# Performance work log

Measured on AMD Instinct MI355X. Metric: run time of the kernel, lower is better.

The kernel has to match this reference:

```python
import jax, jax.numpy as jnp
import numpy as np

B, T, I, H, O = 256, 100, 1024, 2048, 10

def setup_inputs() -> dict:
    key = jax.random.key(0)
    k = jax.random.split(key, 6)
    return {
        "x": jax.random.normal(k[0], (B, T, I), dtype=jnp.float32),
        "h0": jax.random.normal(k[1], (B, H), dtype=jnp.float32),
        "Win": jax.random.uniform(k[2], (I, H), dtype=jnp.float32, minval=-0.1, maxval=0.1),
        "W": jax.random.normal(k[3], (H, H), dtype=jnp.float32) * 0.01,
        "lin_w": jax.random.normal(k[4], (O, H), dtype=jnp.float32) * 0.02,
        "lin_b": jax.random.normal(k[5], (O,), dtype=jnp.float32) * 0.02,
    }

def reference(x, h0, Win, W, lin_w, lin_b):
    xin = jnp.einsum('bti,ih->bth', x, Win)  # precompute input projection for all steps

    def step(h, xin_t):
        h = jnp.tanh(xin_t + h @ W)
        y = h @ lin_w.T + lin_b
        return h, y

    _, ys = jax.lax.scan(step, h0, jnp.swapaxes(xin, 0, 1))  # ys: [T, B, O]
    return jnp.swapaxes(ys, 0, 1)  # [B, T, O]
```

## Files before the change

### kernel.cpp

```cpp
#include <hip/hip_runtime.h>
#include <math.h>

#define Bn 256
#define Tn 100
#define In 1024
#define Hn 2048
#define On 10
#define Kc (In + Hn)

typedef short s8v  __attribute__((ext_vector_type(8)));
typedef unsigned short us4 __attribute__((ext_vector_type(4)));
typedef float f32x4 __attribute__((ext_vector_type(4)));

__device__ __forceinline__ unsigned short f2bf(float f) {
    unsigned int u = __float_as_uint(f);
    u += 0x7fffu + ((u >> 16) & 1u);
    return (unsigned short)(u >> 16);
}


__global__ void conv_x_kernel(const float4* __restrict__ src, ushort4* __restrict__ dst) {
    int i = blockIdx.x * 256 + threadIdx.x;
    float4 v = src[i];
    ushort4 o;
    o.x = f2bf(v.x); o.y = f2bf(v.y); o.z = f2bf(v.z); o.w = f2bf(v.w);
    dst[i] = o;
}

__global__ void transpose_bf16_kernel(const float* __restrict__ src, unsigned short* __restrict__ dst,
                                      int N, int ld, int colOff) {
    __shared__ float tile[32][33];
    int k0 = blockIdx.x * 32;
    int n0 = blockIdx.y * 32;
    int c = threadIdx.x & 31;
    int r = threadIdx.x >> 5;
    #pragma unroll
    for (int i = 0; i < 32; i += 8)
        tile[r + i][c] = src[(size_t)(k0 + r + i) * N + n0 + c];
    __syncthreads();
    #pragma unroll
    for (int i = 0; i < 32; i += 8)
        dst[(size_t)(n0 + r + i) * ld + colOff + k0 + c] = f2bf(tile[c][r + i]);
}

__global__ void small_conv_kernel(const float* __restrict__ h0, const float* __restrict__ lin_w,
                                  unsigned short* __restrict__ h_all0, unsigned short* __restrict__ lwb,
                                  unsigned int* __restrict__ bar) {
    int idx = blockIdx.x * 256 + threadIdx.x;
    if (idx < 512) bar[idx] = 0u;
    if (idx < Bn * Hn) {
        h_all0[idx] = f2bf(h0[idx]);
    } else {
        int j = idx - Bn * Hn;
        int o = j >> 11;
        int k = j & 2047;
        lwb[j] = (o < On) ? f2bf(lin_w[o * Hn + k]) : (unsigned short)0;
    }
}

__global__ __launch_bounds__(512, 2)
void scan_kernel(const unsigned short* __restrict__ xb,
                 const unsigned short* __restrict__ BTm,
                 unsigned short* __restrict__ h_all,
                 unsigned int* __restrict__ bar) {
    const int g = blockIdx.x;
    const int m0 = ((g >> 3) & 3) * 64;
    const int n0 = ((g & 7) * 8 + (g >> 5)) * 32;
    const int w = threadIdx.x >> 6;
    const int lane = threadIdx.x & 63;
    const int quad = lane >> 4;
    const int lr = lane & 15;

    __shared__ float red[4][64][36];

    const unsigned short* bp0 = BTm + (size_t)(n0 + lr) * Kc;
    const unsigned short* bp1 = BTm + (size_t)(n0 + 16 + lr) * Kc;

    const int kbase = w * 384;
    const size_t xrow = (size_t)Tn * In;

    unsigned int* grp_cnt = bar + (g & 7) * 32;
    unsigned int* mst_cnt = bar + 256;
    unsigned int* epoch   = bar + 288;

    for (int t = 0; t < Tn; ++t) {
        f32x4 acc[4][2];
        #pragma unroll
        for (int mi = 0; mi < 4; ++mi)
            #pragma unroll
            for (int ni = 0; ni < 2; ++ni)
                acc[mi][ni] = (f32x4){0.f, 0.f, 0.f, 0.f};

        const unsigned short* hprev = h_all + (size_t)t * (Bn * Hn);
        const unsigned short* xt = xb + (size_t)t * In;

        #pragma unroll
        for (int kk = 0; kk < 12; ++kk) {
            const int k0 = kbase + kk * 32;
            const int kq = k0 + quad * 8;
            const unsigned short* ab;
            size_t rstr;
            if (k0 < In) { ab = xt + kq; rstr = xrow; }
            else         { ab = hprev + (kq - In); rstr = Hn; }
            const unsigned short* arow = ab + (size_t)(m0 + lr) * rstr;
            s8v a0 = *(const s8v*)(arow);
            s8v a1 = *(const s8v*)(arow + 16 * rstr);
            s8v a2 = *(const s8v*)(arow + 32 * rstr);
            s8v a3 = *(const s8v*)(arow + 48 * rstr);
            s8v b0 = *(const s8v*)(bp0 + kq);
            s8v b1 = *(const s8v*)(bp1 + kq);
            acc[0][0] = __builtin_amdgcn_mfma_f32_16x16x32_bf16(a0, b0, acc[0][0], 0, 0, 0);
            acc[1][0] = __builtin_amdgcn_mfma_f32_16x16x32_bf16(a1, b0, acc[1][0], 0, 0, 0);
            acc[2][0] = __builtin_amdgcn_mfma_f32_16x16x32_bf16(a2, b0, acc[2][0], 0, 0, 0);
            acc[3][0] = __builtin_amdgcn_mfma_f32_16x16x32_bf16(a3, b0, acc[3][0], 0, 0, 0);
            acc[0][1] = __builtin_amdgcn_mfma_f32_16x16x32_bf16(a0, b1, acc[0][1], 0, 0, 0);
            acc[1][1] = __builtin_amdgcn_mfma_f32_16x16x32_bf16(a1, b1, acc[1][1], 0, 0, 0);
            acc[2][1] = __builtin_amdgcn_mfma_f32_16x16x32_bf16(a2, b1, acc[2][1], 0, 0, 0);
            acc[3][1] = __builtin_amdgcn_mfma_f32_16x16x32_bf16(a3, b1, acc[3][1], 0, 0, 0);
        }

        if (w < 4) {
            #pragma unroll
            for (int mi = 0; mi < 4; ++mi)
                #pragma unroll
                for (int ni = 0; ni < 2; ++ni)
                    #pragma unroll
                    for (int rr = 0; rr < 4; ++rr)
                        red[w][mi * 16 + quad * 4 + rr][ni * 16 + lr] = acc[mi][ni][rr];
        }
        __syncthreads();
        if (w >= 4) {
            #pragma unroll
            for (int mi = 0; mi < 4; ++mi)
                #pragma unroll
                for (int ni = 0; ni < 2; ++ni)
                    #pragma unroll
                    for (int rr = 0; rr < 4; ++rr)
                        red[w - 4][mi * 16 + quad * 4 + rr][ni * 16 + lr] += acc[mi][ni][rr];
        }
        __syncthreads();

        {
            int j = threadIdx.x << 2;
            int row = j >> 5;
            int c0 = j & 31;
            float4 s0 = *(const float4*)&red[0][row][c0];
            float4 s1 = *(const float4*)&red[1][row][c0];
            float4 s2 = *(const float4*)&red[2][row][c0];
            float4 s3 = *(const float4*)&red[3][row][c0];
            us4 o4;
            o4[0] = f2bf(tanhf(s0.x + s1.x + s2.x + s3.x));
            o4[1] = f2bf(tanhf(s0.y + s1.y + s2.y + s3.y));
            o4[2] = f2bf(tanhf(s0.z + s1.z + s2.z + s3.z));
            o4[3] = f2bf(tanhf(s0.w + s1.w + s2.w + s3.w));
            unsigned long long* dst = (unsigned long long*)
                (h_all + (size_t)(t + 1) * (Bn * Hn) + (size_t)(m0 + row) * Hn + n0 + c0);
            __hip_atomic_store(dst, __builtin_bit_cast(unsigned long long, o4),
                               __ATOMIC_RELAXED, __HIP_MEMORY_SCOPE_AGENT);
        }

        if (t < Tn - 1) {
            __syncthreads();
            if (threadIdx.x == 0) {
                const unsigned int tp1 = (unsigned int)(t + 1);
                unsigned int old = __hip_atomic_fetch_add(grp_cnt, 1u, __ATOMIC_RELAXED,
                                                          __HIP_MEMORY_SCOPE_AGENT);
                if (old == 32u * tp1 - 1u) {
                    unsigned int mo = __hip_atomic_fetch_add(mst_cnt, 1u, __ATOMIC_RELAXED,
                                                             __HIP_MEMORY_SCOPE_AGENT);
                    if (mo == 8u * tp1 - 1u)
                        __hip_atomic_store(epoch, tp1, __ATOMIC_RELAXED,
                                           __HIP_MEMORY_SCOPE_AGENT);
                }
                while (__hip_atomic_load(epoch, __ATOMIC_RELAXED,
                                         __HIP_MEMORY_SCOPE_AGENT) < tp1)
                    __builtin_amdgcn_s_sleep(4);
            }
            __syncthreads();
        }
    }
}

__global__ __launch_bounds__(256)
void gemm2_kernel(const unsigned short* __restrict__ h_all, const unsigned short* __restrict__ lwb,
                  const float* __restrict__ lb, float* __restrict__ y) {
    int gw = blockIdx.x * 4 + (threadIdx.x >> 6);
    int lane = threadIdx.x & 63, quad = lane >> 4, lr = lane & 15;
    int m0 = gw * 16;
    int t = m0 >> 8;
    int b0 = m0 & 255;
    const unsigned short* ah = h_all + ((size_t)(t + 1) * Bn + b0 + lr) * Hn + quad * 8;
    const unsigned short* bh = lwb + (size_t)lr * Hn + quad * 8;
    f32x4 acc0 = {0.f, 0.f, 0.f, 0.f}, acc1 = {0.f, 0.f, 0.f, 0.f};
    #pragma unroll
    for (int k0 = 0; k0 < Hn; k0 += 64) {
        s8v a0 = *(const s8v*)(ah + k0);
        s8v b0 = *(const s8v*)(bh + k0);
        acc0 = __builtin_amdgcn_mfma_f32_16x16x32_bf16(a0, b0, acc0, 0, 0, 0);
        s8v a1 = *(const s8v*)(ah + k0 + 32);
        s8v b1 = *(const s8v*)(bh + k0 + 32);
        acc1 = __builtin_amdgcn_mfma_f32_16x16x32_bf16(a1, b1, acc1, 0, 0, 0);
    }
    acc0 = acc0 + acc1;
    if (lr < On) {
        float bias = lb[lr];
        #pragma unroll
        for (int rr = 0; rr < 4; ++rr) {
            int b = b0 + quad * 4 + rr;
            y[(size_t)b * (Tn * On) + t * On + lr] = acc0[rr] + bias;
        }
    }
}


extern "C" void kernel_launch(void* const* d_in, const int* in_sizes, int n_in,
                              void* d_out, int out_size, void* d_ws, size_t ws_size,
                              hipStream_t stream) {
    const float* x   = (const float*)d_in[0];
    const float* h0  = (const float*)d_in[1];
    const float* Win = (const float*)d_in[2];
    const float* W   = (const float*)d_in[3];
    const float* lw  = (const float*)d_in[4];
    const float* lb  = (const float*)d_in[5];
    float* y = (float*)d_out;

    unsigned short* ws    = (unsigned short*)d_ws;
    unsigned short* xb    = ws;
    unsigned short* BTm   = xb + (size_t)Bn * Tn * In;
    unsigned short* h_all = BTm + (size_t)Hn * Kc;
    unsigned short* lwb   = h_all + (size_t)(Tn + 1) * Bn * Hn;
    unsigned int*   bar   = (unsigned int*)(lwb + 32768);

    conv_x_kernel<<<25600, 256, 0, stream>>>((const float4*)x, (ushort4*)xb);
    transpose_bf16_kernel<<<dim3(32, 64), 256, 0, stream>>>(Win, BTm, Hn, Kc, 0);
    transpose_bf16_kernel<<<dim3(64, 64), 256, 0, stream>>>(W, BTm, Hn, Kc, In);
    small_conv_kernel<<<2176, 256, 0, stream>>>(h0, lw, h_all, lwb, bar);

    scan_kernel<<<256, 512, 0, stream>>>(xb, BTm, h_all, bar);

    gemm2_kernel<<<400, 256, 0, stream>>>(h_all, lwb, lb, y);
}
```

Measured before the change: 1.564 ms.

## Keep weights in registers and overlap next-step input projection with barrier wait

Loads each warp's slice of the concatenated weight matrix into registers once, before the time loop, instead of reloading it every step. The K split is re-partitioned so each warp handles 128 x-columns and 256 h-columns. The x_t·Win contribution for the next step is computed before the grid barrier, so it is not on the serial critical path after the wait. The spin sleep is also shortened. The cost is a large increase in register use (96 extra VGPRs for weights), which may spill or limit occupancy under launch_bounds(512,2).

```diff
diff --git a/kernel.cpp b/kernel.cpp
--- a/kernel.cpp
+++ b/kernel.cpp
@@ -76,47 +76,73 @@
     const unsigned short* bp0 = BTm + (size_t)(n0 + lr) * Kc;
     const unsigned short* bp1 = BTm + (size_t)(n0 + 16 + lr) * Kc;
 
-    const int kbase = w * 384;
     const size_t xrow = (size_t)Tn * In;
 
     unsigned int* grp_cnt = bar + (g & 7) * 32;
     unsigned int* mst_cnt = bar + 256;
     unsigned int* epoch   = bar + 288;
 
+    s8v bx[4][2];
+    s8v bh[8][2];
+    #pragma unroll
+    for (int c = 0; c < 4; ++c) {
+        const int kq = w * 128 + c * 32 + quad * 8;
+        bx[c][0] = *(const s8v*)(bp0 + kq);
+        bx[c][1] = *(const s8v*)(bp1 + kq);
+    }
+    #pragma unroll
+    for (int c = 0; c < 8; ++c) {
+        const int kq = In + w * 256 + c * 32 + quad * 8;
+        bh[c][0] = *(const s8v*)(bp0 + kq);
+        bh[c][1] = *(const s8v*)(bp1 + kq);
+    }
+
+    f32x4 acc[4][2];
+    #pragma unroll
+    for (int mi = 0; mi < 4; ++mi)
+        #pragma unroll
+        for (int ni = 0; ni < 2; ++ni)
+            acc[mi][ni] = (f32x4){0.f, 0.f, 0.f, 0.f};
+
+    {
+        const unsigned short* xt = xb + 0 * In;
+        #pragma unroll
+        for (int c = 0; c < 4; ++c) {
+            const int kq = w * 128 + c * 32 + quad * 8;
+            const unsigned short* arow = xt + kq + (size_t)(m0 + lr) * xrow;
+            s8v a0 = *(const s8v*)(arow);
+            s8v a1 = *(const s8v*)(arow + 16 * xrow);
+            s8v a2 = *(const s8v*)(arow + 32 * xrow);
+            s8v a3 = *(const s8v*)(arow + 48 * xrow);
+            acc[0][0] = __builtin_amdgcn_mfma_f32_16x16x32_bf16(a0, bx[c][0], acc[0][0], 0, 0, 0);
+            acc[1][0] = __builtin_amdgcn_mfma_f32_16x16x32_bf16(a1, bx[c][0], acc[1][0], 0, 0, 0);
+            acc[2][0] = __builtin_amdgcn_mfma_f32_16x16x32_bf16(a2, bx[c][0], acc[2][0], 0, 0, 0);
+            acc[3][0] = __builtin_amdgcn_mfma_f32_16x16x32_bf16(a3, bx[c][0], acc[3][0], 0, 0, 0);
+            acc[0][1] = __builtin_amdgcn_mfma_f32_16x16x32_bf16(a0, bx[c][1], acc[0][1], 0, 0, 0);
+            acc[1][1] = __builtin_amdgcn_mfma_f32_16x16x32_bf16(a1, bx[c][1], acc[1][1], 0, 0, 0);
+            acc[2][1] = __builtin_amdgcn_mfma_f32_16x16x32_bf16(a2, bx[c][1], acc[2][1], 0, 0, 0);
+            acc[3][1] = __builtin_amdgcn_mfma_f32_16x16x32_bf16(a3, bx[c][1], acc[3][1], 0, 0, 0);
+        }
+    }
+
     for (int t = 0; t < Tn; ++t) {
-        f32x4 acc[4][2];
-        #pragma unroll
-        for (int mi = 0; mi < 4; ++mi)
-            #pragma unroll
-            for (int ni = 0; ni < 2; ++ni)
-                acc[mi][ni] = (f32x4){0.f, 0.f, 0.f, 0.f};
-
         const unsigned short* hprev = h_all + (size_t)t * (Bn * Hn);
-        const unsigned short* xt = xb + (size_t)t * In;
-
-        #pragma unroll
-        for (int kk = 0; kk < 12; ++kk) {
-            const int k0 = kbase + kk * 32;
-            const int kq = k0 + quad * 8;
-            const unsigned short* ab;
-            size_t rstr;
-            if (k0 < In) { ab = xt + kq; rstr = xrow; }
-            else         { ab = hprev + (kq - In); rstr = Hn; }
-            const unsigned short* arow = ab + (size_t)(m0 + lr) * rstr;
+        #pragma unroll
+        for (int c = 0; c < 8; ++c) {
+            const int kq = w * 256 + c * 32 + quad * 8;
+            const unsigned short* arow = hprev + kq + (size_t)(m0 + lr) * Hn;
             s8v a0 = *(const s8v*)(arow);
-            s8v a1 = *(const s8v*)(arow + 16 * rstr);
-            s8v a2 = *(const s8v*)(arow + 32 * rstr);
-            s8v a3 = *(const s8v*)(arow + 48 * rstr);
-            s8v b0 = *(const s8v*)(bp0 + kq);
-            s8v b1 = *(const s8v*)(bp1 + kq);
-            acc[0][0] = __builtin_amdgcn_mfma_f32_16x16x32_bf16(a0, b0, acc[0][0], 0, 0, 0);
-            acc[1][0] = __builtin_amdgcn_mfma_f32_16x16x32_bf16(a1, b0, acc[1][0], 0, 0, 0);
-            acc[2][0] = __builtin_amdgcn_mfma_f32_16x16x32_bf16(a2, b0, acc[2][0], 0, 0, 0);
-            acc[3][0] = __builtin_amdgcn_mfma_f32_16x16x32_bf16(a3, b0, acc[3][0], 0, 0, 0);
-            acc[0][1] = __builtin_amdgcn_mfma_f32_16x16x32_bf16(a0, b1, acc[0][1], 0, 0, 0);
-            acc[1][1] = __builtin_amdgcn_mfma_f32_16x16x32_bf16(a1, b1, acc[1][1], 0, 0, 0);
-            acc[2][1] = __builtin_amdgcn_mfma_f32_16x16x32_bf16(a2, b1, acc[2][1], 0, 0, 0);
-            acc[3][1] = __builtin_amdgcn_mfma_f32_16x16x32_bf16(a3, b1, acc[3][1], 0, 0, 0);
+            s8v a1 = *(const s8v*)(arow + 16 * Hn);
+            s8v a2 = *(const s8v*)(arow + 32 * Hn);
+            s8v a3 = *(const s8v*)(arow + 48 * Hn);
+            acc[0][0] = __builtin_amdgcn_mfma_f32_16x16x32_bf16(a0, bh[c][0], acc[0][0], 0, 0, 0);
+            acc[1][0] = __builtin_amdgcn_mfma_f32_16x16x32_bf16(a1, bh[c][0], acc[1][0], 0, 0, 0);
+            acc[2][0] = __builtin_amdgcn_mfma_f32_16x16x32_bf16(a2, bh[c][0], acc[2][0], 0, 0, 0);
+            acc[3][0] = __builtin_amdgcn_mfma_f32_16x16x32_bf16(a3, bh[c][0], acc[3][0], 0, 0, 0);
+            acc[0][1] = __builtin_amdgcn_mfma_f32_16x16x32_bf16(a0, bh[c][1], acc[0][1], 0, 0, 0);
+            acc[1][1] = __builtin_amdgcn_mfma_f32_16x16x32_bf16(a1, bh[c][1], acc[1][1], 0, 0, 0);
+            acc[2][1] = __builtin_amdgcn_mfma_f32_16x16x32_bf16(a2, bh[c][1], acc[2][1], 0, 0, 0);
+            acc[3][1] = __builtin_amdgcn_mfma_f32_16x16x32_bf16(a3, bh[c][1], acc[3][1], 0, 0, 0);
         }
 
         if (w < 4) {
@@ -160,6 +186,30 @@
         }
 
         if (t < Tn - 1) {
+            #pragma unroll
+            for (int mi = 0; mi < 4; ++mi)
+                #pragma unroll
+                for (int ni = 0; ni < 2; ++ni)
+                    acc[mi][ni] = (f32x4){0.f, 0.f, 0.f, 0.f};
+            const unsigned short* xt = xb + (size_t)(t + 1) * In;
+            #pragma unroll
+            for (int c = 0; c < 4; ++c) {
+                const int kq = w * 128 + c * 32 + quad * 8;
+                const unsigned short* arow = xt + kq + (size_t)(m0 + lr) * xrow;
+                s8v a0 = *(const s8v*)(arow);
+                s8v a1 = *(const s8v*)(arow + 16 * xrow);
+                s8v a2 = *(const s8v*)(arow + 32 * xrow);
+                s8v a3 = *(const s8v*)(arow + 48 * xrow);
+                acc[0][0] = __builtin_amdgcn_mfma_f32_16x16x32_bf16(a0, bx[c][0], acc[0][0], 0, 0, 0);
+                acc[1][0] = __builtin_amdgcn_mfma_f32_16x16x32_bf16(a1, bx[c][0], acc[1][0], 0, 0, 0);
+                acc[2][0] = __builtin_amdgcn_mfma_f32_16x16x32_bf16(a2, bx[c][0], acc[2][0], 0, 0, 0);
+                acc[3][0] = __builtin_amdgcn_mfma_f32_16x16x32_bf16(a3, bx[c][0], acc[3][0], 0, 0, 0);
+                acc[0][1] = __builtin_amdgcn_mfma_f32_16x16x32_bf16(a0, bx[c][1], acc[0][1], 0, 0, 0);
+                acc[1][1] = __builtin_amdgcn_mfma_f32_16x16x32_bf16(a1, bx[c][1], acc[1][1], 0, 0, 0);
+                acc[2][1] = __builtin_amdgcn_mfma_f32_16x16x32_bf16(a2, bx[c][1], acc[2][1], 0, 0, 0);
+                acc[3][1] = __builtin_amdgcn_mfma_f32_16x16x32_bf16(a3, bx[c][1], acc[3][1], 0, 0, 0);
+            }
+
             __syncthreads();
             if (threadIdx.x == 0) {
                 const unsigned int tp1 = (unsigned int)(t + 1);
@@ -174,7 +224,7 @@
                 }
                 while (__hip_atomic_load(epoch, __ATOMIC_RELAXED,
                                          __HIP_MEMORY_SCOPE_AGENT) < tp1)
-                    __builtin_amdgcn_s_sleep(4);
+                    __builtin_amdgcn_s_sleep(2);
             }
             __syncthreads();
         }
```

Result: faster. 1.530 ms (-2.2%).
